# Optimization experiments

Hardware: AMD Instinct MI355X
Metric: run time of the kernel (lower is better)

The kernel has to match this reference:

```python
import jax, jax.numpy as jnp
import numpy as np

B, G, N, E, F, H = 16, 8, 512, 8192, 128, 128
BN_EPS = 1e-5


def setup_inputs() -> dict:
    key = jax.random.key(0)
    ks = jax.random.split(key, 6)
    feats = jax.random.normal(ks[0], (B, G, N, F), jnp.float32)
    edges = jax.random.randint(ks[1], (B, G, 2, E), 0, N, dtype=jnp.int32)
    s = lambda k, shape: jax.random.normal(k, shape, jnp.float32) * 0.05
    return {
        "feats": feats,
        "edges": edges,
        "W0": s(ks[2], (F, H)), "b0": jnp.zeros((H,), jnp.float32),
        "W1": s(ks[3], (H, H)), "b1": jnp.zeros((H,), jnp.float32),
        "Wt": s(ks[4], (H, H)), "bt": jnp.zeros((H,), jnp.float32),
        "gamma": jnp.ones((H,), jnp.float32),
        "beta": jnp.zeros((H,), jnp.float32),
        "run_mean": jnp.zeros((H,), jnp.float32),
        "run_var": jnp.ones((H,), jnp.float32),
    }


def _gconv(x, src, dst, W, b):
    # DGL GraphConv with norm='both': relu(D_in^{-1/2} A D_out^{-1/2} X W + b)
    ones = jnp.ones(src.shape, jnp.float32)
    out_deg = jnp.clip(jax.ops.segment_sum(ones, src, num_segments=N), 1.0)
    in_deg = jnp.clip(jax.ops.segment_sum(ones, dst, num_segments=N), 1.0)
    h = x * jax.lax.rsqrt(out_deg)[:, None]          # src normalization
    agg = jax.ops.segment_sum(h[src], dst, num_segments=N)  # SpMM gather+scatter
    h = agg * jax.lax.rsqrt(in_deg)[:, None]          # dst normalization
    return jax.nn.relu(h @ W + b)


def reference(feats, edges, W0, b0, W1, b1, Wt, bt, gamma, beta, run_mean, run_var):
    def per_graph(x, e):
        src, dst = e[0], e[1]
        h = _gconv(x, src, dst, W0, b0)
        h = _gconv(h, src, dst, W1, b1)
        emb = h.mean(axis=0)  # dgl.mean_nodes readout -> [H]
        z = emb @ Wt + bt
        # BatchNorm1d in eval mode (batch of 1 graph embedding)
        z = gamma * (z - run_mean) * jax.lax.rsqrt(run_var + BN_EPS) + beta
        return jax.nn.relu(z)

    xf = feats.reshape(B * G, N, F)
    ef = edges.reshape(B * G, 2, E)
    out = jax.vmap(per_graph)(xf, ef)  # [B*G, H]
    # torch.stack nesting gives (batch, n_graph, 1, H) since mean_nodes returns [1, H]
    return out.reshape(B, G, 1, H)
```

## Files before the change

kernel.cpp:

```cpp
#include <hip/hip_runtime.h>
#include <hip/hip_bf16.h>

#define NN 512
#define NE 8192
#define NG 128
#define FH 128
#define NSEG 64
#define BN_EPS 1e-5f

typedef __attribute__((ext_vector_type(8))) short s8v;
typedef __attribute__((ext_vector_type(4))) float f4v;
typedef __attribute__((ext_vector_type(4))) unsigned short us4v;

__device__ inline void f4acc(float4& a, const float4& b) {
    a.x += b.x; a.y += b.y; a.z += b.z; a.w += b.w;
}

__device__ inline unsigned short f2bf(float x) {
    unsigned u = __float_as_uint(x);
    unsigned r = (u + 0x7fffu + ((u >> 16) & 1u)) >> 16;
    return (unsigned short)r;
}
__device__ inline float bf2f(unsigned short h) { return __uint_as_float(((unsigned)h) << 16); }
__device__ inline float4 bf4_to_f4(const ushort4& v) {
    return make_float4(bf2f(v.x), bf2f(v.y), bf2f(v.z), bf2f(v.w));
}

__global__ __launch_bounds__(1024) void k_build(const int* __restrict__ edges,
                                                float* __restrict__ rs_out,
                                                float* __restrict__ rs_in,
                                                int* __restrict__ row_ofs,
                                                int* __restrict__ csr_src,
                                                int* __restrict__ csr_dst,
                                                int* __restrict__ seg,
                                                const float* __restrict__ W0,
                                                const float* __restrict__ W1,
                                                unsigned short* __restrict__ WP) {
    int g = blockIdx.x;
    int tid = threadIdx.x;

    if (g >= NG) {
        int which = g - NG;
        const float* W = which ? W1 : W0;
        for (int task = tid; task < 2048; task += 1024) {
            int t = task >> 6;
            int lane = task & 63;
            int nt = t >> 2, kk = t & 3;
            int n = nt * 16 + (lane & 15);
            int k0 = kk * 32 + (lane >> 4) * 8;
            unsigned short* dh = WP + ((size_t)which * 2 + 0) * 16384 + ((size_t)t * 64 + lane) * 8;
            unsigned short* dl = WP + ((size_t)which * 2 + 1) * 16384 + ((size_t)t * 64 + lane) * 8;
#pragma unroll
            for (int j = 0; j < 8; j++) {
                float v = W[(size_t)(k0 + j) * FH + n];
                unsigned short h = f2bf(v);
                dh[j] = h;
                dl[j] = f2bf(v - bf2f(h));
            }
        }
        return;
    }

    const int* src = edges + (size_t)g * 2 * NE;
    const int* dst = src + NE;

    __shared__ int degO[NN], degI[NN];
    __shared__ int scanA[NN], scanB[NN];
    __shared__ int fill[NN];
    __shared__ int csr_lds[NE];
    __shared__ int dst_lds[NE];

    for (int i = tid; i < NN; i += 1024) { degO[i] = 0; degI[i] = 0; }
    __syncthreads();
    for (int u = tid; u < NE / 4; u += 1024) {
        int4 s = ((const int4*)src)[u];
        int4 d = ((const int4*)dst)[u];
        atomicAdd(&degO[s.x], 1); atomicAdd(&degO[s.y], 1);
        atomicAdd(&degO[s.z], 1); atomicAdd(&degO[s.w], 1);
        atomicAdd(&degI[d.x], 1); atomicAdd(&degI[d.y], 1);
        atomicAdd(&degI[d.z], 1); atomicAdd(&degI[d.w], 1);
    }
    __syncthreads();
    for (int i = tid; i < NN; i += 1024) {
        int dO = degO[i], dI = degI[i];
        rs_out[g * NN + i] = rsqrtf((float)max(dO, 1));
        rs_in [g * NN + i] = rsqrtf((float)max(dI, 1));
        scanA[i] = dI;
    }
    __syncthreads();
    int* sA = scanA; int* sB = scanB;
    for (int off = 1; off < NN; off <<= 1) {
        for (int i = tid; i < NN; i += 1024) {
            int v = sA[i];
            if (i >= off) v += sA[i - off];
            sB[i] = v;
        }
        __syncthreads();
        int* t = sA; sA = sB; sB = t;
    }
    for (int i = tid; i < NN; i += 1024) {
        int excl = (i == 0) ? 0 : sA[i - 1];
        fill[i] = excl;
        row_ofs[g * 513 + i] = excl;
    }
    if (tid == 0) row_ofs[g * 513 + NN] = sA[NN - 1];
    if (tid < NSEG) {
        int target = tid * (NE / NSEG);
        int lo = 0, hi = NN;
        while (lo < hi) {
            int mid = (lo + hi) >> 1;
            int ex = (mid == 0) ? 0 : sA[mid - 1];
            if (ex >= target) hi = mid; else lo = mid + 1;
        }
        seg[g * (NSEG + 1) + tid] = lo;
    }
    if (tid == 0) seg[g * (NSEG + 1) + NSEG] = NN;
    __syncthreads();
    for (int u = tid; u < NE / 4; u += 1024) {
        int4 s = ((const int4*)src)[u];
        int4 d = ((const int4*)dst)[u];
        int p0 = atomicAdd(&fill[d.x], 1); csr_lds[p0] = s.x; dst_lds[p0] = d.x;
        int p1 = atomicAdd(&fill[d.y], 1); csr_lds[p1] = s.y; dst_lds[p1] = d.y;
        int p2 = atomicAdd(&fill[d.z], 1); csr_lds[p2] = s.z; dst_lds[p2] = d.z;
        int p3 = atomicAdd(&fill[d.w], 1); csr_lds[p3] = s.w; dst_lds[p3] = d.w;
    }
    __syncthreads();
    for (int u = tid; u < NE / 4; u += 1024) {
        ((int4*)(csr_src + (size_t)g * NE))[u] = ((const int4*)csr_lds)[u];
        ((int4*)(csr_dst + (size_t)g * NE))[u] = ((const int4*)dst_lds)[u];
    }
    if (g == NG - 1 && tid < 16) {
        csr_src[(size_t)NG * NE + tid] = 0;
        csr_dst[(size_t)NG * NE + tid] = 0;
    }
}

#define XPITCH 136
__global__ __launch_bounds__(256) void k_gemm_f32(const float* __restrict__ X,
                                                  const unsigned short* __restrict__ WPh,
                                                  const unsigned short* __restrict__ WPl,
                                                  const float* __restrict__ rs,
                                                  unsigned short* __restrict__ Yb) {
    __shared__ unsigned short xh[64 * XPITCH];
    __shared__ unsigned short xl[64 * XPITCH];
    int tid = threadIdx.x;
    size_t r0 = (size_t)blockIdx.x * NN + (size_t)blockIdx.y * 64;

    const float4* Xv = (const float4*)(X + r0 * FH);
#pragma unroll
    for (int i = 0; i < 8; i++) {
        int u = tid + i * 256;
        int row = u >> 5, c4 = (u & 31) * 4;
        float4 v = Xv[u];
        int off = row * XPITCH + c4;
        unsigned short h0 = f2bf(v.x), h1 = f2bf(v.y), h2 = f2bf(v.z), h3 = f2bf(v.w);
        xh[off + 0] = h0; xh[off + 1] = h1; xh[off + 2] = h2; xh[off + 3] = h3;
        xl[off + 0] = f2bf(v.x - bf2f(h0));
        xl[off + 1] = f2bf(v.y - bf2f(h1));
        xl[off + 2] = f2bf(v.z - bf2f(h2));
        xl[off + 3] = f2bf(v.w - bf2f(h3));
    }
    __syncthreads();

    int lane = tid & 63, w = tid >> 6;
    int quad = lane >> 4, m = lane & 15;
    int arow = w * 16 + m;

    f4v acc[8];
#pragma unroll
    for (int nt = 0; nt < 8; nt++) acc[nt] = (f4v){0.f, 0.f, 0.f, 0.f};

#pragma unroll
    for (int kk = 0; kk < 4; kk++) {
        s8v ah = *(const s8v*)&xh[arow * XPITCH + kk * 32 + quad * 8];
        s8v al = *(const s8v*)&xl[arow * XPITCH + kk * 32 + quad * 8];
#pragma unroll
        for (int nt = 0; nt < 8; nt++) {
            s8v bh = *(const s8v*)(WPh + ((size_t)(nt * 4 + kk) * 64 + lane) * 8);
            s8v bl = *(const s8v*)(WPl + ((size_t)(nt * 4 + kk) * 64 + lane) * 8);
            acc[nt] = __builtin_amdgcn_mfma_f32_16x16x32_bf16(ah, bh, acc[nt], 0, 0, 0);
            acc[nt] = __builtin_amdgcn_mfma_f32_16x16x32_bf16(al, bh, acc[nt], 0, 0, 0);
            acc[nt] = __builtin_amdgcn_mfma_f32_16x16x32_bf16(ah, bl, acc[nt], 0, 0, 0);
        }
    }

    int orow = w * 16 + quad * 4;
    float4 rsv = *(const float4*)(rs + r0 + orow);
#pragma unroll
    for (int nt = 0; nt < 8; nt++) {
        Yb[(r0 + orow + 0) * FH + nt * 16 + m] = f2bf(acc[nt][0] * rsv.x);
        Yb[(r0 + orow + 1) * FH + nt * 16 + m] = f2bf(acc[nt][1] * rsv.y);
        Yb[(r0 + orow + 2) * FH + nt * 16 + m] = f2bf(acc[nt][2] * rsv.z);
        Yb[(r0 + orow + 3) * FH + nt * 16 + m] = f2bf(acc[nt][3] * rsv.w);
    }
}

__global__ __launch_bounds__(256) void k_gemm_bf16(const unsigned short* __restrict__ X,
                                                   const unsigned short* __restrict__ WPh,
                                                   const unsigned short* __restrict__ WPl,
                                                   const float* __restrict__ rs,
                                                   unsigned short* __restrict__ Yb) {
    __shared__ unsigned short xh[64 * XPITCH];
    int tid = threadIdx.x;
    size_t r0 = (size_t)blockIdx.x * NN + (size_t)blockIdx.y * 64;

    const ushort4* Xv = (const ushort4*)(X + r0 * FH);
#pragma unroll
    for (int i = 0; i < 8; i++) {
        int u = tid + i * 256;
        int row = u >> 5, c4 = (u & 31) * 4;
        ushort4 v = Xv[u];
        int off = row * XPITCH + c4;
        xh[off + 0] = v.x; xh[off + 1] = v.y; xh[off + 2] = v.z; xh[off + 3] = v.w;
    }
    __syncthreads();

    int lane = tid & 63, w = tid >> 6;
    int quad = lane >> 4, m = lane & 15;
    int arow = w * 16 + m;

    f4v acc[8];
#pragma unroll
    for (int nt = 0; nt < 8; nt++) acc[nt] = (f4v){0.f, 0.f, 0.f, 0.f};

#pragma unroll
    for (int kk = 0; kk < 4; kk++) {
        s8v ah = *(const s8v*)&xh[arow * XPITCH + kk * 32 + quad * 8];
#pragma unroll
        for (int nt = 0; nt < 8; nt++) {
            s8v bh = *(const s8v*)(WPh + ((size_t)(nt * 4 + kk) * 64 + lane) * 8);
            s8v bl = *(const s8v*)(WPl + ((size_t)(nt * 4 + kk) * 64 + lane) * 8);
            acc[nt] = __builtin_amdgcn_mfma_f32_16x16x32_bf16(ah, bh, acc[nt], 0, 0, 0);
            acc[nt] = __builtin_amdgcn_mfma_f32_16x16x32_bf16(ah, bl, acc[nt], 0, 0, 0);
        }
    }

    int orow = w * 16 + quad * 4;
    float4 rsv = *(const float4*)(rs + r0 + orow);
#pragma unroll
    for (int nt = 0; nt < 8; nt++) {
        Yb[(r0 + orow + 0) * FH + nt * 16 + m] = f2bf(acc[nt][0] * rsv.x);
        Yb[(r0 + orow + 1) * FH + nt * 16 + m] = f2bf(acc[nt][1] * rsv.y);
        Yb[(r0 + orow + 2) * FH + nt * 16 + m] = f2bf(acc[nt][2] * rsv.z);
        Yb[(r0 + orow + 3) * FH + nt * 16 + m] = f2bf(acc[nt][3] * rsv.w);
    }
}

__global__ __launch_bounds__(256) void k_gather(const unsigned short* __restrict__ Yb,
                                                const int* __restrict__ row_ofs,
                                                const int* __restrict__ csr_src,
                                                const int* __restrict__ csr_dst,
                                                const int* __restrict__ seg,
                                                const float* __restrict__ rs_in,
                                                const float* __restrict__ bias,
                                                unsigned short* __restrict__ H) {
    int g  = blockIdx.x;
    int sb = blockIdx.y;
    int tid = threadIdx.x;
    int lane = tid & 31;
    int grp  = tid >> 5;

    __shared__ float rsin_s[NN];
    for (int i = tid; i < NN; i += 256) rsin_s[i] = rs_in[g * NN + i];
    __syncthreads();

    int sidx = sb * 8 + grp;
    int d0 = seg[g * (NSEG + 1) + sidx], d1 = seg[g * (NSEG + 1) + sidx + 1];
    if (d0 >= d1) return;

    const int* ro = row_ofs + g * 513;
    const ushort4* Yv = (const ushort4*)(Yb + (size_t)g * NN * FH);
    const int* cs = csr_src + (size_t)g * NE;
    const int* cd = csr_dst + (size_t)g * NE;
    int e0 = ro[d0], eEnd = ro[d1];
    float4 bv = ((const float4*)bias)[lane];
    us4v rbn;
    rbn.x = f2bf(fmaxf(bv.x, 0.f)); rbn.y = f2bf(fmaxf(bv.y, 0.f));
    rbn.z = f2bf(fmaxf(bv.z, 0.f)); rbn.w = f2bf(fmaxf(bv.w, 0.f));
    us4v* Hg = (us4v*)(H + (size_t)g * NN * FH) + lane;

    int d = d0;
    float4 acc = make_float4(0.f, 0.f, 0.f, 0.f);
    int e = e0 & ~3;
    int4 S0 = *(const int4*)(cs + e),     D0 = *(const int4*)(cd + e);
    int4 S1 = *(const int4*)(cs + e + 4), D1 = *(const int4*)(cd + e + 4);
    ushort4 y0 = Yv[S0.x * 32 + lane];
    ushort4 y1 = Yv[S0.y * 32 + lane];
    ushort4 y2 = Yv[S0.z * 32 + lane];
    ushort4 y3 = Yv[S0.w * 32 + lane];
    for (; e < eEnd; e += 4) {
        int4 S2 = *(const int4*)(cs + e + 8);
        int4 D2 = *(const int4*)(cd + e + 8);
        ushort4 z0 = Yv[S1.x * 32 + lane];
        ushort4 z1 = Yv[S1.y * 32 + lane];
        ushort4 z2 = Yv[S1.z * 32 + lane];
        ushort4 z3 = Yv[S1.w * 32 + lane];
#define STEP(J, DJ, YJ)                                                     \
        {                                                                   \
            int idx = e + (J);                                              \
            bool valid = (idx >= e0) & (idx < eEnd);                        \
            if (valid && (DJ) != d) {                                       \
                float r = rsin_s[d];                                        \
                us4v h;                                                     \
                h.x = f2bf(fmaxf(fmaf(r, acc.x, bv.x), 0.f));               \
                h.y = f2bf(fmaxf(fmaf(r, acc.y, bv.y), 0.f));               \
                h.z = f2bf(fmaxf(fmaf(r, acc.z, bv.z), 0.f));               \
                h.w = f2bf(fmaxf(fmaf(r, acc.w, bv.w), 0.f));               \
                __builtin_nontemporal_store(h, Hg + (size_t)d * 32);        \
                for (int dd = d + 1; dd < (DJ); dd++)                       \
                    __builtin_nontemporal_store(rbn, Hg + (size_t)dd * 32); \
                d = (DJ);                                                   \
                acc = make_float4(0.f, 0.f, 0.f, 0.f);                      \
            }                                                               \
            if (valid) f4acc(acc, bf4_to_f4(YJ));                           \
        }
        STEP(0, D0.x, y0) STEP(1, D0.y, y1) STEP(2, D0.z, y2) STEP(3, D0.w, y3)
#undef STEP
        S0 = S1; D0 = D1; S1 = S2; D1 = D2;
        y0 = z0; y1 = z1; y2 = z2; y3 = z3;
    }
    {
        float r = rsin_s[d];
        us4v h;
        h.x = f2bf(fmaxf(fmaf(r, acc.x, bv.x), 0.f));
        h.y = f2bf(fmaxf(fmaf(r, acc.y, bv.y), 0.f));
        h.z = f2bf(fmaxf(fmaf(r, acc.z, bv.z), 0.f));
        h.w = f2bf(fmaxf(fmaf(r, acc.w, bv.w), 0.f));
        __builtin_nontemporal_store(h, Hg + (size_t)d * 32);
        for (int dd = d + 1; dd < d1; dd++)
            __builtin_nontemporal_store(rbn, Hg + (size_t)dd * 32);
    }
}

__global__ __launch_bounds__(256) void k_gather_mean(const unsigned short* __restrict__ Yb,
                                                     const int* __restrict__ row_ofs,
                                                     const int* __restrict__ csr_src,
                                                     const int* __restrict__ csr_dst,
                                                     const int* __restrict__ seg,
                                                     const float* __restrict__ rs_in,
                                                     const float* __restrict__ bias,
                                                     float* __restrict__ partial) {
    int g  = blockIdx.x;
    int sb = blockIdx.y;
    int tid = threadIdx.x;
    int lane = tid & 31;
    int grp  = tid >> 5;

    __shared__ float rsin_s[NN];
    __shared__ float4 red[8][32];
    for (int i = tid; i < NN; i += 256) rsin_s[i] = rs_in[g * NN + i];
    __syncthreads();

    int sidx = sb * 8 + grp;
    int d0 = seg[g * (NSEG + 1) + sidx], d1 = seg[g * (NSEG + 1) + sidx + 1];

    const int* ro = row_ofs + g * 513;
    const ushort4* Yv = (const ushort4*)(Yb + (size_t)g * NN * FH);
    const int* cs = csr_src + (size_t)g * NE;
    const int* cd = csr_dst + (size_t)g * NE;
    float4 bv = ((const float4*)bias)[lane];
    float4 rb;
    rb.x = fmaxf(bv.x, 0.f); rb.y = fmaxf(bv.y, 0.f);
    rb.z = fmaxf(bv.z, 0.f); rb.w = fmaxf(bv.w, 0.f);

    float4 sum = make_float4(0.f, 0.f, 0.f, 0.f);
    if (d0 < d1) {
        int e0 = ro[d0], eEnd = ro[d1];
        int d = d0;
        float4 acc = make_float4(0.f, 0.f, 0.f, 0.f);
        int e = e0 & ~3;
        int4 S0 = *(const int4*)(cs + e),     D0 = *(const int4*)(cd + e);
        int4 S1 = *(const int4*)(cs + e + 4), D1 = *(const int4*)(cd + e + 4);
        ushort4 y0 = Yv[S0.x * 32 + lane];
        ushort4 y1 = Yv[S0.y * 32 + lane];
        ushort4 y2 = Yv[S0.z * 32 + lane];
        ushort4 y3 = Yv[S0.w * 32 + lane];
        for (; e < eEnd; e += 4) {
            int4 S2 = *(const int4*)(cs + e + 8);
            int4 D2 = *(const int4*)(cd + e + 8);
            ushort4 z0 = Yv[S1.x * 32 + lane];
            ushort4 z1 = Yv[S1.y * 32 + lane];
            ushort4 z2 = Yv[S1.z * 32 + lane];
            ushort4 z3 = Yv[S1.w * 32 + lane];
#define STEP(J, DJ, YJ)                                                     \
            {                                                               \
                int idx = e + (J);                                          \
                bool valid = (idx >= e0) & (idx < eEnd);                    \
                if (valid && (DJ) != d) {                                   \
                    float r = rsin_s[d];                                    \
                    sum.x += fmaxf(fmaf(r, acc.x, bv.x), 0.f);              \
                    sum.y += fmaxf(fmaf(r, acc.y, bv.y), 0.f);              \
                    sum.z += fmaxf(fmaf(r, acc.z, bv.z), 0.f);              \
                    sum.w += fmaxf(fmaf(r, acc.w, bv.w), 0.f);              \
                    float gf = (float)((DJ) - d - 1);                       \
                    sum.x += gf * rb.x; sum.y += gf * rb.y;                 \
                    sum.z += gf * rb.z; sum.w += gf * rb.w;                 \
                    d = (DJ);                                               \
                    acc = make_float4(0.f, 0.f, 0.f, 0.f);                  \
                }                                                           \
                if (valid) f4acc(acc, bf4_to_f4(YJ));                       \
            }
            STEP(0, D0.x, y0) STEP(1, D0.y, y1) STEP(2, D0.z, y2) STEP(3, D0.w, y3)
#undef STEP
            S0 = S1; D0 = D1; S1 = S2; D1 = D2;
            y0 = z0; y1 = z1; y2 = z2; y3 = z3;
        }
        {
            float r = rsin_s[d];
            sum.x += fmaxf(fmaf(r, acc.x, bv.x), 0.f);
            sum.y += fmaxf(fmaf(r, acc.y, bv.y), 0.f);
            sum.z += fmaxf(fmaf(r, acc.z, bv.z), 0.f);
            sum.w += fmaxf(fmaf(r, acc.w, bv.w), 0.f);
            float gf = (float)(d1 - 1 - d);
            sum.x += gf * rb.x; sum.y += gf * rb.y;
            sum.z += gf * rb.z; sum.w += gf * rb.w;
        }
    }

    red[grp][lane] = sum;
    __syncthreads();
    if (grp == 0) {
        float4 t = red[0][lane];
#pragma unroll
        for (int j = 1; j < 8; j++) f4acc(t, red[j][lane]);
        *(float4*)(partial + (((size_t)g * 8 + sb) * FH) + lane * 4) = t;
    }
}

__global__ __launch_bounds__(128) void k_head(const float* __restrict__ partial,
                                              const float* __restrict__ Wt,
                                              const float* __restrict__ bt,
                                              const float* __restrict__ gamma,
                                              const float* __restrict__ beta,
                                              const float* __restrict__ rmean,
                                              const float* __restrict__ rvar,
                                              float* __restrict__ out) {
    int g = blockIdx.x;
    int j = threadIdx.x;
    __shared__ float e[FH];
    float acc8 = 0.f;
#pragma unroll
    for (int q = 0; q < 8; q++) acc8 += partial[((size_t)g * 8 + q) * FH + j];
    e[j] = acc8 * (1.0f / (float)NN);
    __syncthreads();
    float acc = bt[j];
#pragma unroll 8
    for (int k = 0; k < FH; k++) acc += e[k] * Wt[(size_t)k * FH + j];
    float z = gamma[j] * (acc - rmean[j]) * rsqrtf(rvar[j] + BN_EPS) + beta[j];
    out[g * FH + j] = fmaxf(z, 0.f);
}

extern "C" void kernel_launch(void* const* d_in, const int* in_sizes, int n_in,
                              void* d_out, int out_size, void* d_ws, size_t ws_size,
                              hipStream_t stream) {
    const float* feats = (const float*)d_in[0];
    const int*   edges = (const int*)d_in[1];
    const float* W0    = (const float*)d_in[2];
    const float* b0    = (const float*)d_in[3];
    const float* W1    = (const float*)d_in[4];
    const float* b1    = (const float*)d_in[5];
    const float* Wt    = (const float*)d_in[6];
    const float* bt    = (const float*)d_in[7];
    const float* gamma = (const float*)d_in[8];
    const float* beta  = (const float*)d_in[9];
    const float* rmean = (const float*)d_in[10];
    const float* rvar  = (const float*)d_in[11];
    float* out = (float*)d_out;

    char* w = (char*)d_ws;
    float* rs_out  = (float*)w;   w += sizeof(float) * NG * NN;
    float* rs_in   = (float*)w;   w += sizeof(float) * NG * NN;
    int*   row_ofs = (int*)w;     w += sizeof(int) * NG * 520;
    int*   seg     = (int*)w;     w += sizeof(int) * NG * (NSEG + 1) + 64;
    int*   csr_src = (int*)w;     w += sizeof(int) * ((size_t)NG * NE + 16);
    int*   csr_dst = (int*)w;     w += sizeof(int) * ((size_t)NG * NE + 16);
    unsigned short* WP = (unsigned short*)w;  w += sizeof(unsigned short) * 4 * 16384;
    unsigned short* Yb  = (unsigned short*)w; w += sizeof(unsigned short) * (size_t)NG * NN * FH;
    unsigned short* H1b = (unsigned short*)w; w += sizeof(unsigned short) * (size_t)NG * NN * FH;
    float* partial = (float*)w;   w += sizeof(float) * NG * 8 * FH;

    unsigned short* WPh0 = WP;
    unsigned short* WPl0 = WP + 16384;
    unsigned short* WPh1 = WP + 32768;
    unsigned short* WPl1 = WP + 49152;

    k_build<<<NG + 2, 1024, 0, stream>>>(edges, rs_out, rs_in, row_ofs, csr_src, csr_dst, seg,
                                         W0, W1, WP);

    k_gemm_f32<<<dim3(NG, 8), 256, 0, stream>>>(feats, WPh0, WPl0, rs_out, Yb);

    k_gather<<<dim3(NG, 8), 256, 0, stream>>>(Yb, row_ofs, csr_src, csr_dst, seg, rs_in, b0, H1b);

    k_gemm_bf16<<<dim3(NG, 8), 256, 0, stream>>>(H1b, WPh1, WPl1, rs_out, Yb);

    k_gather_mean<<<dim3(NG, 8), 256, 0, stream>>>(Yb, row_ofs, csr_src, csr_dst, seg, rs_in, b1, partial);

    k_head<<<NG, 128, 0, stream>>>(partial, Wt, bt, gamma, beta, rmean, rvar, out);

    (void)in_sizes; (void)n_in; (void)out_size; (void)ws_size;
}
```

Baseline: 199.8 us.

## Fuse first-layer gather with second GEMM via slab-aligned segments in LDS

Merges the first SpMM gather and the second bf16 GEMM into one kernel. Each block aggregates its 64 destination rows into shared memory and then runs the MFMA GEMM directly on that tile, so the H1 intermediate never round-trips through global memory and one launch is removed. To make this work, segment boundaries are recomputed so each group of 8 segments stays within its 64-row slab, trading global edge balance for balance within each slab. Per-block load may become uneven when edge counts differ between slabs.

```diff
diff --git a/kernel.cpp b/kernel.cpp
--- a/kernel.cpp
+++ b/kernel.cpp
@@ -105,8 +105,12 @@
     }
     if (tid == 0) row_ofs[g * 513 + NN] = sA[NN - 1];
     if (tid < NSEG) {
-        int target = tid * (NE / NSEG);
-        int lo = 0, hi = NN;
+        int sb = tid >> 3, j = tid & 7;
+        int base_row = sb * 64;
+        int cumB = (base_row == 0) ? 0 : sA[base_row - 1];
+        int slabE = sA[base_row + 63] - cumB;
+        int target = cumB + (j * slabE) / 8;
+        int lo = base_row, hi = base_row + 64;
         while (lo < hi) {
             int mid = (lo + hi) >> 1;
             int ex = (mid == 0) ? 0 : sA[mid - 1];
@@ -195,140 +199,129 @@
     }
 }
 
-__global__ __launch_bounds__(256) void k_gemm_bf16(const unsigned short* __restrict__ X,
-                                                   const unsigned short* __restrict__ WPh,
-                                                   const unsigned short* __restrict__ WPl,
-                                                   const float* __restrict__ rs,
-                                                   unsigned short* __restrict__ Yb) {
-    __shared__ unsigned short xh[64 * XPITCH];
-    int tid = threadIdx.x;
-    size_t r0 = (size_t)blockIdx.x * NN + (size_t)blockIdx.y * 64;
-
-    const ushort4* Xv = (const ushort4*)(X + r0 * FH);
-#pragma unroll
-    for (int i = 0; i < 8; i++) {
-        int u = tid + i * 256;
-        int row = u >> 5, c4 = (u & 31) * 4;
-        ushort4 v = Xv[u];
-        int off = row * XPITCH + c4;
-        xh[off + 0] = v.x; xh[off + 1] = v.y; xh[off + 2] = v.z; xh[off + 3] = v.w;
-    }
-    __syncthreads();
-
-    int lane = tid & 63, w = tid >> 6;
-    int quad = lane >> 4, m = lane & 15;
-    int arow = w * 16 + m;
-
-    f4v acc[8];
-#pragma unroll
-    for (int nt = 0; nt < 8; nt++) acc[nt] = (f4v){0.f, 0.f, 0.f, 0.f};
-
-#pragma unroll
-    for (int kk = 0; kk < 4; kk++) {
-        s8v ah = *(const s8v*)&xh[arow * XPITCH + kk * 32 + quad * 8];
-#pragma unroll
-        for (int nt = 0; nt < 8; nt++) {
-            s8v bh = *(const s8v*)(WPh + ((size_t)(nt * 4 + kk) * 64 + lane) * 8);
-            s8v bl = *(const s8v*)(WPl + ((size_t)(nt * 4 + kk) * 64 + lane) * 8);
-            acc[nt] = __builtin_amdgcn_mfma_f32_16x16x32_bf16(ah, bh, acc[nt], 0, 0, 0);
-            acc[nt] = __builtin_amdgcn_mfma_f32_16x16x32_bf16(ah, bl, acc[nt], 0, 0, 0);
-        }
-    }
-
-    int orow = w * 16 + quad * 4;
-    float4 rsv = *(const float4*)(rs + r0 + orow);
-#pragma unroll
-    for (int nt = 0; nt < 8; nt++) {
-        Yb[(r0 + orow + 0) * FH + nt * 16 + m] = f2bf(acc[nt][0] * rsv.x);
-        Yb[(r0 + orow + 1) * FH + nt * 16 + m] = f2bf(acc[nt][1] * rsv.y);
-        Yb[(r0 + orow + 2) * FH + nt * 16 + m] = f2bf(acc[nt][2] * rsv.z);
-        Yb[(r0 + orow + 3) * FH + nt * 16 + m] = f2bf(acc[nt][3] * rsv.w);
-    }
-}
-
-__global__ __launch_bounds__(256) void k_gather(const unsigned short* __restrict__ Yb,
-                                                const int* __restrict__ row_ofs,
-                                                const int* __restrict__ csr_src,
-                                                const int* __restrict__ csr_dst,
-                                                const int* __restrict__ seg,
-                                                const float* __restrict__ rs_in,
-                                                const float* __restrict__ bias,
-                                                unsigned short* __restrict__ H) {
+__global__ __launch_bounds__(256) void k_fused(const unsigned short* __restrict__ Y1,
+                                               const int* __restrict__ row_ofs,
+                                               const int* __restrict__ csr_src,
+                                               const int* __restrict__ csr_dst,
+                                               const int* __restrict__ seg,
+                                               const float* __restrict__ rs_in,
+                                               const float* __restrict__ rs_out,
+                                               const float* __restrict__ bias,
+                                               const unsigned short* __restrict__ WPh,
+                                               const unsigned short* __restrict__ WPl,
+                                               unsigned short* __restrict__ Y2) {
     int g  = blockIdx.x;
     int sb = blockIdx.y;
     int tid = threadIdx.x;
     int lane = tid & 31;
     int grp  = tid >> 5;
-
-    __shared__ float rsin_s[NN];
-    for (int i = tid; i < NN; i += 256) rsin_s[i] = rs_in[g * NN + i];
+    int base = sb * 64;
+
+    __shared__ unsigned short hs[64 * XPITCH];
+    __shared__ float rsin_s[64];
+
+    if (tid < 64) rsin_s[tid] = rs_in[g * NN + base + tid];
     __syncthreads();
 
     int sidx = sb * 8 + grp;
     int d0 = seg[g * (NSEG + 1) + sidx], d1 = seg[g * (NSEG + 1) + sidx + 1];
-    if (d0 >= d1) return;
-
-    const int* ro = row_ofs + g * 513;
-    const ushort4* Yv = (const ushort4*)(Yb + (size_t)g * NN * FH);
-    const int* cs = csr_src + (size_t)g * NE;
-    const int* cd = csr_dst + (size_t)g * NE;
-    int e0 = ro[d0], eEnd = ro[d1];
-    float4 bv = ((const float4*)bias)[lane];
-    us4v rbn;
-    rbn.x = f2bf(fmaxf(bv.x, 0.f)); rbn.y = f2bf(fmaxf(bv.y, 0.f));
-    rbn.z = f2bf(fmaxf(bv.z, 0.f)); rbn.w = f2bf(fmaxf(bv.w, 0.f));
-    us4v* Hg = (us4v*)(H + (size_t)g * NN * FH) + lane;
-
-    int d = d0;
-    float4 acc = make_float4(0.f, 0.f, 0.f, 0.f);
-    int e = e0 & ~3;
-    int4 S0 = *(const int4*)(cs + e),     D0 = *(const int4*)(cd + e);
-    int4 S1 = *(const int4*)(cs + e + 4), D1 = *(const int4*)(cd + e + 4);
-    ushort4 y0 = Yv[S0.x * 32 + lane];
-    ushort4 y1 = Yv[S0.y * 32 + lane];
-    ushort4 y2 = Yv[S0.z * 32 + lane];
-    ushort4 y3 = Yv[S0.w * 32 + lane];
-    for (; e < eEnd; e += 4) {
-        int4 S2 = *(const int4*)(cs + e + 8);
-        int4 D2 = *(const int4*)(cd + e + 8);
-        ushort4 z0 = Yv[S1.x * 32 + lane];
-        ushort4 z1 = Yv[S1.y * 32 + lane];
-        ushort4 z2 = Yv[S1.z * 32 + lane];
-        ushort4 z3 = Yv[S1.w * 32 + lane];
+
+    {
+        const int* ro = row_ofs + g * 513;
+        const ushort4* Yv = (const ushort4*)(Y1 + (size_t)g * NN * FH);
+        const int* cs = csr_src + (size_t)g * NE;
+        const int* cd = csr_dst + (size_t)g * NE;
+        float4 bv = ((const float4*)bias)[lane];
+        us4v rbn;
+        rbn.x = f2bf(fmaxf(bv.x, 0.f)); rbn.y = f2bf(fmaxf(bv.y, 0.f));
+        rbn.z = f2bf(fmaxf(bv.z, 0.f)); rbn.w = f2bf(fmaxf(bv.w, 0.f));
+
+        if (d0 < d1) {
+            int e0 = ro[d0], eEnd = ro[d1];
+            int d = d0;
+            float4 acc = make_float4(0.f, 0.f, 0.f, 0.f);
+            int e = e0 & ~3;
+            int4 S0 = *(const int4*)(cs + e),     D0 = *(const int4*)(cd + e);
+            int4 S1 = *(const int4*)(cs + e + 4), D1 = *(const int4*)(cd + e + 4);
+            ushort4 y0 = Yv[S0.x * 32 + lane];
+            ushort4 y1 = Yv[S0.y * 32 + lane];
+            ushort4 y2 = Yv[S0.z * 32 + lane];
+            ushort4 y3 = Yv[S0.w * 32 + lane];
+            for (; e < eEnd; e += 4) {
+                int4 S2 = *(const int4*)(cs + e + 8);
+                int4 D2 = *(const int4*)(cd + e + 8);
+                ushort4 z0 = Yv[S1.x * 32 + lane];
+                ushort4 z1 = Yv[S1.y * 32 + lane];
+                ushort4 z2 = Yv[S1.z * 32 + lane];
+                ushort4 z3 = Yv[S1.w * 32 + lane];
 #define STEP(J, DJ, YJ)                                                     \
-        {                                                                   \
-            int idx = e + (J);                                              \
-            bool valid = (idx >= e0) & (idx < eEnd);                        \
-            if (valid && (DJ) != d) {                                       \
-                float r = rsin_s[d];                                        \
-                us4v h;                                                     \
-                h.x = f2bf(fmaxf(fmaf(r, acc.x, bv.x), 0.f));               \
-                h.y = f2bf(fmaxf(fmaf(r, acc.y, bv.y), 0.f));               \
-                h.z = f2bf(fmaxf(fmaf(r, acc.z, bv.z), 0.f));               \
-                h.w = f2bf(fmaxf(fmaf(r, acc.w, bv.w), 0.f));               \
-                __builtin_nontemporal_store(h, Hg + (size_t)d * 32);        \
-                for (int dd = d + 1; dd < (DJ); dd++)                       \
-                    __builtin_nontemporal_store(rbn, Hg + (size_t)dd * 32); \
-                d = (DJ);                                                   \
-                acc = make_float4(0.f, 0.f, 0.f, 0.f);                      \
-            }                                                               \
-            if (valid) f4acc(acc, bf4_to_f4(YJ));                           \
-        }
-        STEP(0, D0.x, y0) STEP(1, D0.y, y1) STEP(2, D0.z, y2) STEP(3, D0.w, y3)
+                {                                                           \
+                    int idx = e + (J);                                      \
+                    bool valid = (idx >= e0) & (idx < eEnd);                \
+                    if (valid && (DJ) != d) {                               \
+                        float r = rsin_s[d - base];                         \
+                        us4v h;                                             \
+                        h.x = f2bf(fmaxf(fmaf(r, acc.x, bv.x), 0.f));       \
+                        h.y = f2bf(fmaxf(fmaf(r, acc.y, bv.y), 0.f));       \
+                        h.z = f2bf(fmaxf(fmaf(r, acc.z, bv.z), 0.f));       \
+                        h.w = f2bf(fmaxf(fmaf(r, acc.w, bv.w), 0.f));       \
+                        *(us4v*)&hs[(d - base) * XPITCH + lane * 4] = h;    \
+                        for (int dd = d + 1; dd < (DJ); dd++)               \
+                            *(us4v*)&hs[(dd - base) * XPITCH + lane * 4] = rbn; \
+                        d = (DJ);                                           \
+                        acc = make_float4(0.f, 0.f, 0.f, 0.f);              \
+                    }                                                       \
+                    if (valid) f4acc(acc, bf4_to_f4(YJ));                   \
+                }
+                STEP(0, D0.x, y0) STEP(1, D0.y, y1) STEP(2, D0.z, y2) STEP(3, D0.w, y3)
 #undef STEP
-        S0 = S1; D0 = D1; S1 = S2; D1 = D2;
-        y0 = z0; y1 = z1; y2 = z2; y3 = z3;
-    }
-    {
-        float r = rsin_s[d];
-        us4v h;
-        h.x = f2bf(fmaxf(fmaf(r, acc.x, bv.x), 0.f));
-        h.y = f2bf(fmaxf(fmaf(r, acc.y, bv.y), 0.f));
-        h.z = f2bf(fmaxf(fmaf(r, acc.z, bv.z), 0.f));
-        h.w = f2bf(fmaxf(fmaf(r, acc.w, bv.w), 0.f));
-        __builtin_nontemporal_store(h, Hg + (size_t)d * 32);
-        for (int dd = d + 1; dd < d1; dd++)
-            __builtin_nontemporal_store(rbn, Hg + (size_t)dd * 32);
+                S0 = S1; D0 = D1; S1 = S2; D1 = D2;
+                y0 = z0; y1 = z1; y2 = z2; y3 = z3;
+            }
+            {
+                float r = rsin_s[d - base];
+                us4v h;
+                h.x = f2bf(fmaxf(fmaf(r, acc.x, bv.x), 0.f));
+                h.y = f2bf(fmaxf(fmaf(r, acc.y, bv.y), 0.f));
+                h.z = f2bf(fmaxf(fmaf(r, acc.z, bv.z), 0.f));
+                h.w = f2bf(fmaxf(fmaf(r, acc.w, bv.w), 0.f));
+                *(us4v*)&hs[(d - base) * XPITCH + lane * 4] = h;
+                for (int dd = d + 1; dd < d1; dd++)
+                    *(us4v*)&hs[(dd - base) * XPITCH + lane * 4] = rbn;
+            }
+        }
+    }
+    __syncthreads();
+
+    int lane64 = tid & 63, w = tid >> 6;
+    int quad = lane64 >> 4, m = lane64 & 15;
+    int arow = w * 16 + m;
+    size_t r0 = (size_t)g * NN + base;
+
+    f4v acc[8];
+#pragma unroll
+    for (int nt = 0; nt < 8; nt++) acc[nt] = (f4v){0.f, 0.f, 0.f, 0.f};
+
+#pragma unroll
+    for (int kk = 0; kk < 4; kk++) {
+        s8v ah = *(const s8v*)&hs[arow * XPITCH + kk * 32 + quad * 8];
+#pragma unroll
+        for (int nt = 0; nt < 8; nt++) {
+            s8v bh = *(const s8v*)(WPh + ((size_t)(nt * 4 + kk) * 64 + lane64) * 8);
+            s8v bl = *(const s8v*)(WPl + ((size_t)(nt * 4 + kk) * 64 + lane64) * 8);
+            acc[nt] = __builtin_amdgcn_mfma_f32_16x16x32_bf16(ah, bh, acc[nt], 0, 0, 0);
+            acc[nt] = __builtin_amdgcn_mfma_f32_16x16x32_bf16(ah, bl, acc[nt], 0, 0, 0);
+        }
+    }
+
+    int orow = w * 16 + quad * 4;
+    float4 rsv = *(const float4*)(rs_out + r0 + orow);
+#pragma unroll
+    for (int nt = 0; nt < 8; nt++) {
+        Y2[(r0 + orow + 0) * FH + nt * 16 + m] = f2bf(acc[nt][0] * rsv.x);
+        Y2[(r0 + orow + 1) * FH + nt * 16 + m] = f2bf(acc[nt][1] * rsv.y);
+        Y2[(r0 + orow + 2) * FH + nt * 16 + m] = f2bf(acc[nt][2] * rsv.z);
+        Y2[(r0 + orow + 3) * FH + nt * 16 + m] = f2bf(acc[nt][3] * rsv.w);
     }
 }
 
@@ -475,8 +468,8 @@
     int*   csr_src = (int*)w;     w += sizeof(int) * ((size_t)NG * NE + 16);
     int*   csr_dst = (int*)w;     w += sizeof(int) * ((size_t)NG * NE + 16);
     unsigned short* WP = (unsigned short*)w;  w += sizeof(unsigned short) * 4 * 16384;
-    unsigned short* Yb  = (unsigned short*)w; w += sizeof(unsigned short) * (size_t)NG * NN * FH;
-    unsigned short* H1b = (unsigned short*)w; w += sizeof(unsigned short) * (size_t)NG * NN * FH;
+    unsigned short* Y1 = (unsigned short*)w;  w += sizeof(unsigned short) * (size_t)NG * NN * FH;
+    unsigned short* Y2 = (unsigned short*)w;  w += sizeof(unsigned short) * (size_t)NG * NN * FH;
     float* partial = (float*)w;   w += sizeof(float) * NG * 8 * FH;
 
     unsigned short* WPh0 = WP;
@@ -487,13 +480,12 @@
     k_build<<<NG + 2, 1024, 0, stream>>>(edges, rs_out, rs_in, row_ofs, csr_src, csr_dst, seg,
                                          W0, W1, WP);
 
-    k_gemm_f32<<<dim3(NG, 8), 256, 0, stream>>>(feats, WPh0, WPl0, rs_out, Yb);
-
-    k_gather<<<dim3(NG, 8), 256, 0, stream>>>(Yb, row_ofs, csr_src, csr_dst, seg, rs_in, b0, H1b);
-
-    k_gemm_bf16<<<dim3(NG, 8), 256, 0, stream>>>(H1b, WPh1, WPl1, rs_out, Yb);
-
-    k_gather_mean<<<dim3(NG, 8), 256, 0, stream>>>(Yb, row_ofs, csr_src, csr_dst, seg, rs_in, b1, partial);
+    k_gemm_f32<<<dim3(NG, 8), 256, 0, stream>>>(feats, WPh0, WPl0, rs_out, Y1);
+
+    k_fused<<<dim3(NG, 8), 256, 0, stream>>>(Y1, row_ofs, csr_src, csr_dst, seg,
+                                             rs_in, rs_out, b0, WPh1, WPl1, Y2);
+
+    k_gather_mean<<<dim3(NG, 8), 256, 0, stream>>>(Y2, row_ofs, csr_src, csr_dst, seg, rs_in, b1, partial);
 
     k_head<<<NG, 128, 0, stream>>>(partial, Wt, bt, gamma, beta, rmean, rvar, out);
 
```

Result: faster. 194.0 us (-2.9%).
